# Performance work log

Hardware: AMD Instinct MI355X
Metric: run time of the kernel (lower is better)

## Reference

```python
import jax, jax.numpy as jnp
import numpy as np

B, S, D, H, L = 32, 512, 256, 8, 3
HD = D // H
FFN = D // 2
SCALE_BASE = 512.0
EPS = 1e-5


def _gammas():
    return (1.0 - jnp.exp(jnp.linspace(np.log(1.0 / 32.0), np.log(1.0 / 512.0), H))).astype(jnp.float32)


def _xpos(x, downscale):
    # x: [..., S, hd]; XPOS rotary embedding with exponential length scaling
    s, hd = x.shape[-2], x.shape[-1]
    half = hd // 2
    scale = (jnp.arange(0, hd, 2, dtype=jnp.float32) + 0.4 * hd) / (1.4 * hd)  # [half]
    power = jnp.arange(s, dtype=jnp.float32)[:, None] / SCALE_BASE
    sm = scale[None, :] ** power  # [S, half]
    if downscale:
        sm = 1.0 / sm
    inv_freq = 1.0 / (10000.0 ** (jnp.arange(half, dtype=jnp.float32) / half))
    ang = jnp.arange(s, dtype=jnp.float32)[:, None] * inv_freq[None, :]  # [S, half]
    sin = jnp.repeat(jnp.sin(ang) * sm, 2, axis=-1)  # duplicate_interleave -> [S, hd]
    cos = jnp.repeat(jnp.cos(ang) * sm, 2, axis=-1)
    x1, x2 = x[..., ::2], x[..., 1::2]
    rot = jnp.stack((-x2, x1), axis=-1).reshape(x.shape)  # rotate_every_two
    return x * cos + rot * sin


def _layer_norm(x, w, b):
    mu = x.mean(-1, keepdims=True)
    var = ((x - mu) ** 2).mean(-1, keepdims=True)
    return (x - mu) / jnp.sqrt(var + EPS) * w + b


def _msr(X, WQ, WK, WV, WG, WO, gn_w, gn_b):
    # Multi-scale retention, parallel form. X: [B,S,D]; WQ/WK/WV: [H,D,HD]
    b, s, _ = X.shape
    Q = _xpos(jnp.einsum('bsd,hde->bhse', X, WQ), False)
    K = _xpos(jnp.einsum('bsd,hde->bhse', X, WK), True)
    V = jnp.einsum('bsd,hde->bhse', X, WV)
    n = jnp.arange(s)
    delta = (n[:, None] - n[None, :]).astype(jnp.float32)
    mask = n[:, None] >= n[None, :]
    g = _gammas()
    Dm = jnp.where(mask[None], g[:, None, None] ** delta[None], 0.0)  # [H,S,S]
    scores = jnp.einsum('bhse,bhte->bhst', Q, K) * Dm[None]  # [B,H,S,S]
    Y = jnp.einsum('bhst,bhte->bhse', scores, V)  # [B,H,S,HD]
    Y = jnp.moveaxis(Y, 1, 2)  # [B,S,H,HD] (= concat heads)
    # GroupNorm(heads, v_dim): normalize per (token, head) group
    mu = Y.mean(-1, keepdims=True)
    var = ((Y - mu) ** 2).mean(-1, keepdims=True)
    Yn = ((Y - mu) / jnp.sqrt(var + EPS)).reshape(b, s, D) * gn_w + gn_b
    G = X @ WG
    return (G * jax.nn.sigmoid(G) * Yn) @ WO


def setup_inputs() -> dict:
    key = jax.random.key(0)
    ks = jax.random.split(key, 10)
    inp = {
        'v': jax.random.randint(ks[0], (B, S), 0, 65, dtype=jnp.int64),
        'emb': jax.random.normal(ks[1], (65, D), dtype=jnp.float32),
        'WQ': jax.random.normal(ks[2], (L, H, D, HD), dtype=jnp.float32) / D,
        'WK': jax.random.normal(ks[3], (L, H, D, HD), dtype=jnp.float32) / D,
        'WV': jax.random.normal(ks[4], (L, H, D, HD), dtype=jnp.float32) / D,
        'WG': jax.random.normal(ks[5], (L, D, D), dtype=jnp.float32) / D,
        'WO': jax.random.normal(ks[6], (L, D, D), dtype=jnp.float32) / D,
        'gn_w': jnp.ones((L, D), jnp.float32),
        'gn_b': jnp.zeros((L, D), jnp.float32),
        'ln1_w': jnp.ones((L, D), jnp.float32),
        'ln1_b': jnp.zeros((L, D), jnp.float32),
        'ln2_w': jnp.ones((L, D), jnp.float32),
        'ln2_b': jnp.zeros((L, D), jnp.float32),
        'w1': jax.random.normal(ks[7], (L, D, FFN), dtype=jnp.float32) * (1.0 / np.sqrt(D)),
        'b1': jnp.zeros((L, FFN), jnp.float32),
        'w2': jax.random.normal(ks[8], (L, FFN, D), dtype=jnp.float32) * (1.0 / np.sqrt(FFN)),
        'b2': jnp.zeros((L, D), jnp.float32),
    }
    return inp


def reference(v, emb, WQ, WK, WV, WG, WO, gn_w, gn_b, ln1_w, ln1_b, ln2_w, ln2_b, w1, b1, w2, b2):
    emb = emb.at[0].set(0.0)  # padding_idx=0
    X = jax.nn.relu(emb[v])  # [B,S,D]
    for i in range(L):
        Y = _msr(_layer_norm(X, ln1_w[i], ln1_b[i]), WQ[i], WK[i], WV[i], WG[i], WO[i], gn_w[i], gn_b[i]) + X
        h = jax.nn.gelu(_layer_norm(Y, ln2_w[i], ln2_b[i]) @ w1[i] + b1[i], approximate=False)
        X = h @ w2[i] + b2[i] + Y
    return X
```

## Files before the change

### kernel.cpp

```cpp
#include <hip/hip_runtime.h>
#include <hip/hip_bf16.h>
#include <math.h>

#define BB 32
#define SS 512
#define DD 256
#define HH 8
#define HDIM 32
#define FFNN 128
#define NROWS (BB*SS)
#define NELEM (NROWS*DD)

using bf16 = __hip_bfloat16;
typedef __attribute__((ext_vector_type(8))) short short8;
typedef __attribute__((ext_vector_type(4))) short short4v;
typedef __attribute__((ext_vector_type(4))) float floatx4;
typedef unsigned int uint_al __attribute__((may_alias));

static __device__ __forceinline__ float bf2f(bf16 x) { return __bfloat162float(x); }
static __device__ __forceinline__ bf16  f2bf(float x) { return __float2bfloat16(x); }
static __device__ __forceinline__ short f2bfs(float x) {
    bf16 b = __float2bfloat16(x);
    return __builtin_bit_cast(short, b);
}

static __device__ __forceinline__ unsigned int cvtpk(float a, float b) {
    unsigned int r;
    asm("v_cvt_pk_bf16_f32 %0, %1, %2" : "=v"(r) : "v"(a), "v"(b));
    return r;
}
static __device__ __forceinline__ short4v mk4(unsigned int a, unsigned int b) {
    union { unsigned int u[2]; short4v s; } t;
    t.u[0] = a; t.u[1] = b;
    return t.s;
}
static __device__ __forceinline__ floatx4 mfma16(short4v a, short4v b, floatx4 c) {
#if __has_builtin(__builtin_amdgcn_mfma_f32_16x16x16bf16_1k)
    return __builtin_amdgcn_mfma_f32_16x16x16bf16_1k(a, b, c, 0, 0, 0);
#else
    asm("v_mfma_f32_16x16x16_bf16 %0, %1, %2, %0" : "+v"(c) : "v"(a), "v"(b));
    return c;
#endif
}

static __device__ __forceinline__ void gld_lds16(const void* g, void* l) {
    __builtin_amdgcn_global_load_lds(
        (const __attribute__((address_space(1))) void*)g,
        (__attribute__((address_space(3))) void*)l, 16, 0, 0);
}

__global__ void init_flag(int* flag) { *flag = 0; }
__global__ __launch_bounds__(256) void detect_v(const int* __restrict__ v, int* __restrict__ flag) {
    int i = blockIdx.x * 256 + threadIdx.x;
    if (v[2 * i + 1] != 0) atomicOr(flag, 1);
}

#define NQKVG (3*1024*256)
#define NWO   (3*256*256)
#define NW1   (3*128*256)
#define NW2   (3*256*128)
#define NXPT  (512*16)
#define NSETUP (NQKVG+NWO+NW1+NW2+NXPT)
__global__ __launch_bounds__(256) void setup_pack(const float* __restrict__ WQ, const float* __restrict__ WK,
                                                  const float* __restrict__ WV, const float* __restrict__ WG,
                                                  const float* __restrict__ WO, const float* __restrict__ w1,
                                                  const float* __restrict__ w2,
                                                  bf16* __restrict__ dQ, bf16* __restrict__ dO,
                                                  bf16* __restrict__ d1, bf16* __restrict__ d2,
                                                  float4* __restrict__ xpt) {
    int idx = blockIdx.x * 256 + threadIdx.x;
    if (idx < NQKVG) {
        int k = idx & 255, n = (idx >> 8) & 1023, l = idx >> 18;
        int seg = n >> 8, n8 = n & 255;
        float val;
        if (seg < 3) {
            const float* W = (seg == 0) ? WQ : (seg == 1) ? WK : WV;
            int h = n8 >> 5, e = n8 & 31;
            val = W[(((size_t)l * 8 + h) * 256 + k) * 32 + e];
        } else {
            val = WG[(size_t)l * 65536 + k * 256 + n8];
        }
        dQ[((size_t)l * 1024 + n) * 256 + k] = f2bf(val);
    } else if (idx < NQKVG + NWO) {
        int i = idx - NQKVG;
        int k = i & 255, n = (i >> 8) & 255, l = i >> 16;
        dO[((size_t)l * 256 + n) * 256 + k] = f2bf(WO[(size_t)l * 65536 + k * 256 + n]);
    } else if (idx < NQKVG + NWO + NW1) {
        int i = idx - NQKVG - NWO;
        int k = i & 255, n = (i >> 8) & 127, l = i >> 15;
        d1[((size_t)l * 128 + n) * 256 + k] = f2bf(w1[(size_t)l * 32768 + k * 128 + n]);
    } else if (idx < NQKVG + NWO + NW1 + NW2) {
        int i = idx - NQKVG - NWO - NW1;
        int k = i & 127, n = (i >> 7) & 255, l = i >> 15;
        d2[((size_t)l * 256 + n) * 128 + k] = f2bf(w2[(size_t)l * 32768 + k * 256 + n]);
    } else {
        int i = idx - NQKVG - NWO - NW1 - NW2;
        int jf = i & 15, s = i >> 4;
        float base = (2.0f * jf + 12.8f) / 44.8f;
        float sm = powf(base, (float)s * (1.0f / 512.0f));
        float ang = (float)s * powf(10000.0f, -(float)jf / 16.0f);
        float sn, cs;
        sincosf(ang, &sn, &cs);
        xpt[i] = float4{cs * sm, sn * sm, cs / sm, sn / sm};
    }
}

__global__ __launch_bounds__(256) void embed_ln_kernel(const int* __restrict__ v,
                                                       const float* __restrict__ emb,
                                                       const int* __restrict__ flag,
                                                       const float* __restrict__ w,
                                                       const float* __restrict__ b,
                                                       float* __restrict__ X,
                                                       short* __restrict__ Xn) {
    int row = blockIdx.x;
    int d = threadIdx.x;
    int tok = (*flag) ? v[row] : v[2 * row];
    float x = 0.0f;
    if (tok != 0) {
        x = emb[tok * DD + d];
        x = x > 0.0f ? x : 0.0f;
    }
    X[(size_t)row * DD + d] = x;
    float s1 = x, s2 = x * x;
    #pragma unroll
    for (int off = 1; off < 64; off <<= 1) {
        s1 += __shfl_xor(s1, off);
        s2 += __shfl_xor(s2, off);
    }
    __shared__ float p1[4], p2[4], st[2];
    int wid = threadIdx.x >> 6;
    if ((threadIdx.x & 63) == 0) { p1[wid] = s1; p2[wid] = s2; }
    __syncthreads();
    if (threadIdx.x == 0) {
        float t1 = p1[0] + p1[1] + p1[2] + p1[3];
        float t2 = p2[0] + p2[1] + p2[2] + p2[3];
        float mu = t1 * (1.0f / DD);
        float var = t2 * (1.0f / DD) - mu * mu;
        st[0] = mu; st[1] = rsqrtf(var + 1e-5f);
    }
    __syncthreads();
    Xn[(size_t)row * DD + d] = f2bfs((x - st[0]) * st[1] * w[d] + b[d]);
}

__global__ __launch_bounds__(256) void qkvg_gemm(const short* __restrict__ A,
                                                 const short* __restrict__ Bp,
                                                 const float4* __restrict__ xpt,
                                                 bf16* __restrict__ C) {
    __shared__ __align__(16) short Als[16 * 512];
    __shared__ __align__(16) short Bls[16 * 512];
    const int tid = threadIdx.x;
    const int wave = tid >> 6, lane = tid & 63, lo = lane & 15, quad = lane >> 4;
    const int wm = wave >> 1, wn = wave & 1;
    const int row0 = blockIdx.x * 128, col0 = blockIdx.y * 128;

    floatx4 acc[4][4];
    #pragma unroll
    for (int i = 0; i < 4; ++i)
        #pragma unroll
        for (int j = 0; j < 4; ++j) acc[i][j] = floatx4{0.f, 0.f, 0.f, 0.f};

    for (int k0 = 0; k0 < 256; k0 += 64) {
        #pragma unroll
        for (int t = 0; t < 4; ++t) {
            int grp = (wm * 4 + t) * 2 + wn;
            const short* ga = A + (size_t)(row0 + (wm * 4 + t) * 16 + lo) * 256
                            + k0 + (wn * 4 + quad) * 8;
            gld_lds16(ga, &Als[grp * 512]);
        }
        #pragma unroll
        for (int t = 0; t < 4; ++t) {
            int grp = (wn * 4 + t) * 2 + wm;
            const short* gb = Bp + (size_t)(col0 + (wn * 4 + t) * 16 + lo) * 256
                            + k0 + (wm * 4 + quad) * 8;
            gld_lds16(gb, &Bls[grp * 512]);
        }
        __syncthreads();
        #pragma unroll
        for (int kkgrp = 0; kkgrp < 2; ++kkgrp) {
            short8 af[4], bfr[4];
            #pragma unroll
            for (int t = 0; t < 4; ++t)
                af[t] = *(const short8*)(&Als[((wm * 4 + t) * 2 + kkgrp) * 512 + lane * 8]);
            #pragma unroll
            for (int t = 0; t < 4; ++t)
                bfr[t] = *(const short8*)(&Bls[((wn * 4 + t) * 2 + kkgrp) * 512 + lane * 8]);
            #pragma unroll
            for (int ti = 0; ti < 4; ++ti)
                #pragma unroll
                for (int tj = 0; tj < 4; ++tj)
                    acc[ti][tj] = __builtin_amdgcn_mfma_f32_16x16x32_bf16(af[ti], bfr[tj], acc[ti][tj], 0, 0, 0);
        }
        __syncthreads();
    }

    #pragma unroll
    for (int ti = 0; ti < 4; ++ti) {
        #pragma unroll
        for (int tj = 0; tj < 4; ++tj) {
            int colb = col0 + (wn * 4 + tj) * 16 + lo;
            int seg = colb >> 8;
            #pragma unroll
            for (int r = 0; r < 4; ++r) {
                int row = row0 + (wm * 4 + ti) * 16 + quad * 4 + r;
                float v = acc[ti][tj][r];
                if (seg < 2) {
                    int s = row & (SS - 1);
                    int jf = (colb & 31) >> 1;
                    float4 t = xpt[s * 16 + jf];
                    float cs = (seg == 0) ? t.x : t.z;
                    float sn = (seg == 0) ? t.y : t.w;
                    float p = __shfl_xor(v, 1);
                    v = (lo & 1) ? (v * cs + p * sn) : (v * cs - p * sn);
                }
                C[(size_t)row * 1024 + colb] = f2bf(v);
            }
        }
    }
}

#define HS2 264
#define HSTR 136
template<int DOLN>
__global__ __launch_bounds__(256) void wo_ffn_fused(const short* __restrict__ A,
                                                    const short* __restrict__ Wo,
                                                    const short* __restrict__ W1p,
                                                    const float* __restrict__ b1,
                                                    const short* __restrict__ W2p,
                                                    const float* __restrict__ b2,
                                                    float* __restrict__ X,
                                                    const float* __restrict__ ln2w,
                                                    const float* __restrict__ ln2b,
                                                    const float* __restrict__ ln1w,
                                                    const float* __restrict__ ln1b,
                                                    short* __restrict__ Xn) {
    __shared__ __align__(16) short Als[4 * 512];
    __shared__ __align__(16) short Bls[4][8 * 512];
    __shared__ __align__(16) short Hn[32 * HS2];
    __shared__ __align__(16) short Hf[32 * HSTR];
    __shared__ float Ssum[32][4], Ssq[32][4];
    const int tid = threadIdx.x;
    const int wave = tid >> 6, lane = tid & 63, lo = lane & 15, quad = lane >> 4;
    const int row0 = blockIdx.x * 32;
    const int colw0 = wave * 64;

    floatx4 acc[2][4];
    #pragma unroll
    for (int i = 0; i < 2; ++i)
        #pragma unroll
        for (int j = 0; j < 4; ++j) acc[i][j] = floatx4{0.f, 0.f, 0.f, 0.f};

    const short* Ab = A + (size_t)(row0 + (wave >> 1) * 16 + lo) * 1024 + ((wave & 1) * 4 + quad) * 8;
    const short* Bb = Wo + (size_t)(colw0 + lo) * 256 + quad * 8;

    for (int k0 = 0; k0 < 256; k0 += 64) {
        gld_lds16(Ab + k0, &Als[wave * 512]);
        #pragma unroll
        for (int t = 0; t < 4; ++t)
            #pragma unroll
            for (int kk = 0; kk < 2; ++kk)
                gld_lds16(Bb + (size_t)(t * 16) * 256 + k0 + kk * 32,
                          &Bls[wave][(t * 2 + kk) * 512]);
        __syncthreads();
        #pragma unroll
        for (int kk = 0; kk < 2; ++kk) {
            short8 af[2], bfr[4];
            #pragma unroll
            for (int t = 0; t < 2; ++t)
                af[t] = *(const short8*)(&Als[(t * 2 + kk) * 512 + lane * 8]);
            #pragma unroll
            for (int t = 0; t < 4; ++t)
                bfr[t] = *(const short8*)(&Bls[wave][(t * 2 + kk) * 512 + lane * 8]);
            #pragma unroll
            for (int ti = 0; ti < 2; ++ti)
                #pragma unroll
                for (int tj = 0; tj < 4; ++tj)
                    acc[ti][tj] = __builtin_amdgcn_mfma_f32_16x16x32_bf16(af[ti], bfr[tj], acc[ti][tj], 0, 0, 0);
        }
        __syncthreads();
    }

    float vv[2][4][4];
    #pragma unroll
    for (int ti = 0; ti < 2; ++ti)
        #pragma unroll
        for (int tj = 0; tj < 4; ++tj) {
            int colb = colw0 + tj * 16 + lo;
            #pragma unroll
            for (int r = 0; r < 4; ++r) {
                int row = row0 + ti * 16 + quad * 4 + r;
                vv[ti][tj][r] = acc[ti][tj][r] + X[(size_t)row * DD + colb];
            }
        }
    #pragma unroll
    for (int ti = 0; ti < 2; ++ti)
        #pragma unroll
        for (int r = 0; r < 4; ++r) {
            float s1 = 0.f, s2 = 0.f;
            #pragma unroll
            for (int tj = 0; tj < 4; ++tj) {
                float v = vv[ti][tj][r];
                s1 += v; s2 += v * v;
            }
            #pragma unroll
            for (int off = 1; off < 16; off <<= 1) {
                s1 += __shfl_xor(s1, off);
                s2 += __shfl_xor(s2, off);
            }
            if (lo == 0) {
                int rl = ti * 16 + quad * 4 + r;
                Ssum[rl][wave] = s1;
                Ssq[rl][wave] = s2;
            }
        }
    __syncthreads();
    #pragma unroll
    for (int ti = 0; ti < 2; ++ti)
        #pragma unroll
        for (int r = 0; r < 4; ++r) {
            int rl = ti * 16 + quad * 4 + r;
            float t1 = Ssum[rl][0] + Ssum[rl][1] + Ssum[rl][2] + Ssum[rl][3];
            float t2 = Ssq[rl][0] + Ssq[rl][1] + Ssq[rl][2] + Ssq[rl][3];
            float mu = t1 * (1.0f / DD);
            float var = t2 * (1.0f / DD) - mu * mu;
            float rs = rsqrtf(var + 1e-5f);
            #pragma unroll
            for (int tj = 0; tj < 4; ++tj) {
                int colb = colw0 + tj * 16 + lo;
                Hn[rl * HS2 + colb] =
                    f2bfs((vv[ti][tj][r] - mu) * rs * ln2w[colb] + ln2b[colb]);
            }
        }
    __syncthreads();

    floatx4 a1[2][2];
    #pragma unroll
    for (int i = 0; i < 2; ++i) { a1[i][0] = floatx4{0,0,0,0}; a1[i][1] = floatx4{0,0,0,0}; }
    const short* Bb1 = W1p + (size_t)(wave * 32 + lo) * 256 + quad * 8;
    for (int k0 = 0; k0 < 256; k0 += 64) {
        #pragma unroll
        for (int t = 0; t < 2; ++t)
            #pragma unroll
            for (int kk = 0; kk < 2; ++kk)
                gld_lds16(Bb1 + (size_t)(t * 16) * 256 + k0 + kk * 32,
                          &Bls[wave][(t * 2 + kk) * 512]);
        __syncthreads();
        #pragma unroll
        for (int kk = 0; kk < 2; ++kk) {
            short8 af[2], bfr[2];
            #pragma unroll
            for (int t = 0; t < 2; ++t)
                af[t] = *(const short8*)(&Hn[(t * 16 + lo) * HS2 + k0 + kk * 32 + quad * 8]);
            #pragma unroll
            for (int t = 0; t < 2; ++t)
                bfr[t] = *(const short8*)(&Bls[wave][(t * 2 + kk) * 512 + lane * 8]);
            #pragma unroll
            for (int ti = 0; ti < 2; ++ti)
                #pragma unroll
                for (int tj = 0; tj < 2; ++tj)
                    a1[ti][tj] = __builtin_amdgcn_mfma_f32_16x16x32_bf16(af[ti], bfr[tj], a1[ti][tj], 0, 0, 0);
        }
        __syncthreads();
    }
    #pragma unroll
    for (int ti = 0; ti < 2; ++ti)
        #pragma unroll
        for (int tj = 0; tj < 2; ++tj) {
            int colb = wave * 32 + tj * 16 + lo;
            float bs = b1[colb];
            #pragma unroll
            for (int r = 0; r < 4; ++r) {
                int rl = ti * 16 + quad * 4 + r;
                float v = a1[ti][tj][r] + bs;
                v = 0.5f * v * (1.0f + erff(v * 0.70710678118f));
                Hf[rl * HSTR + colb] = f2bfs(v);
            }
        }

    floatx4 a2[2][4];
    #pragma unroll
    for (int i = 0; i < 2; ++i)
        #pragma unroll
        for (int j = 0; j < 4; ++j) a2[i][j] = floatx4{0,0,0,0};
    const short* Bb2 = W2p + (size_t)(colw0 + lo) * 128 + quad * 8;
    for (int k0 = 0; k0 < 128; k0 += 64) {
        #pragma unroll
        for (int t = 0; t < 4; ++t)
            #pragma unroll
            for (int kk = 0; kk < 2; ++kk)
                gld_lds16(Bb2 + (size_t)(t * 16) * 128 + k0 + kk * 32,
                          &Bls[wave][(t * 2 + kk) * 512]);
        __syncthreads();
        #pragma unroll
        for (int kk = 0; kk < 2; ++kk) {
            short8 af[2], bfr[4];
            #pragma unroll
            for (int t = 0; t < 2; ++t)
                af[t] = *(const short8*)(&Hf[(t * 16 + lo) * HSTR + k0 + kk * 32 + quad * 8]);
            #pragma unroll
            for (int t = 0; t < 4; ++t)
                bfr[t] = *(const short8*)(&Bls[wave][(t * 2 + kk) * 512 + lane * 8]);
            #pragma unroll
            for (int ti = 0; ti < 2; ++ti)
                #pragma unroll
                for (int tj = 0; tj < 4; ++tj)
                    a2[ti][tj] = __builtin_amdgcn_mfma_f32_16x16x32_bf16(af[ti], bfr[tj], a2[ti][tj], 0, 0, 0);
        }
        __syncthreads();
    }

    #pragma unroll
    for (int ti = 0; ti < 2; ++ti)
        #pragma unroll
        for (int tj = 0; tj < 4; ++tj) {
            int colb = colw0 + tj * 16 + lo;
            float bs = b2[colb];
            #pragma unroll
            for (int r = 0; r < 4; ++r) {
                int row = row0 + ti * 16 + quad * 4 + r;
                float v = a2[ti][tj][r] + bs + vv[ti][tj][r];
                X[(size_t)row * DD + colb] = v;
                vv[ti][tj][r] = v;
            }
        }
    if (!DOLN) return;
    #pragma unroll
    for (int ti = 0; ti < 2; ++ti)
        #pragma unroll
        for (int r = 0; r < 4; ++r) {
            float s1 = 0.f, s2 = 0.f;
            #pragma unroll
            for (int tj = 0; tj < 4; ++tj) {
                float v = vv[ti][tj][r];
                s1 += v; s2 += v * v;
            }
            #pragma unroll
            for (int off = 1; off < 16; off <<= 1) {
                s1 += __shfl_xor(s1, off);
                s2 += __shfl_xor(s2, off);
            }
            if (lo == 0) {
                int rl = ti * 16 + quad * 4 + r;
                Ssum[rl][wave] = s1;
                Ssq[rl][wave] = s2;
            }
        }
    __syncthreads();
    #pragma unroll
    for (int ti = 0; ti < 2; ++ti)
        #pragma unroll
        for (int r = 0; r < 4; ++r) {
            int rl = ti * 16 + quad * 4 + r;
            float t1 = Ssum[rl][0] + Ssum[rl][1] + Ssum[rl][2] + Ssum[rl][3];
            float t2 = Ssq[rl][0] + Ssq[rl][1] + Ssq[rl][2] + Ssq[rl][3];
            float mu = t1 * (1.0f / DD);
            float var = t2 * (1.0f / DD) - mu * mu;
            float rs = rsqrtf(var + 1e-5f);
            int row = row0 + rl;
            #pragma unroll
            for (int tj = 0; tj < 4; ++tj) {
                int colb = colw0 + tj * 16 + lo;
                Xn[(size_t)row * DD + colb] =
                    f2bfs((vv[ti][tj][r] - mu) * rs * ln1w[colb] + ln1b[colb]);
            }
        }
}

#define VSTR 44
__global__ __launch_bounds__(256) void retention_mfma_kernel(bf16* __restrict__ QKVG,
                                                             const float* __restrict__ gnw,
                                                             const float* __restrict__ gnb) {
    __shared__ __align__(16) short Vt[4][32 * VSTR];
    const int wslot = threadIdx.x >> 6;
    const int lane = threadIdx.x & 63;
    const int gblk = blockIdx.x >> 6;
    const int qi = 15 - ((gblk & ~3) + (((gblk & 3) + (gblk >> 2)) & 3));
    const int bh = ((blockIdx.x & 63) << 2) | wslot;
    const int b = bh >> 3, h = bh & 7;
    const int q0 = qi * 32;
    const int lo = lane & 15, quad = lane >> 4;

    const float la0 = -3.46573590280f, la1 = -6.23832462504f;
    float gamma = 1.0f - expf(la0 + (float)h * (la1 - la0) / 7.0f);
    float lg2 = log2f(gamma);
    float g16i = exp2f(-16.0f * lg2);
    float g16p = exp2f(16.0f * lg2);
    float gi32 = exp2f(-32.0f * lg2);
    float wq[4], wq16[4], wqB[4];
    #pragma unroll
    for (int r = 0; r < 4; ++r) {
        wq[r]   = exp2f((float)(lo - 4 * quad - r) * lg2);
        wq16[r] = wq[r] * g16i;
        wqB[r]  = wq[r] * g16p;
    }
    float c = exp2f((float)q0 * lg2);

    const size_t base = (size_t)b * SS * 1024;
    const short* QKVGs = (const short*)QKVG;

    short8 qfA = *(const short8*)(QKVGs + base + (size_t)(q0 + lo) * 1024 + h * HDIM + quad * 8);
    short8 qfB = *(const short8*)(QKVGs + base + (size_t)(q0 + 16 + lo) * 1024 + h * HDIM + quad * 8);

    floatx4 oA0 = {0,0,0,0}, oA1 = {0,0,0,0}, oB0 = {0,0,0,0}, oB1 = {0,0,0,0};
    short* Vw = Vt[wslot];
    const int nch = qi + 1;

    for (int ch = 0; ch < nch; ++ch) {
        const int t0 = ch * 32;
        const short* Kb = QKVGs + base + 256 + h * HDIM + quad * 8;
        short8 kf0 = *(const short8*)(Kb + (size_t)(t0 + lo) * 1024);
        short8 kf1 = *(const short8*)(Kb + (size_t)(t0 + 16 + lo) * 1024);
        {
            const int r = lane >> 2, dcol = (lane & 3) * 8;
            const short* Vg = QKVGs + base + 512 + h * HDIM + dcol;
            uint4 u1 = *(const uint4*)(Vg + (size_t)(t0 + r) * 1024);
            uint4 u2 = *(const uint4*)(Vg + (size_t)(t0 + 16 + r) * 1024);
            uint_al* W1 = (uint_al*)(Vw + r * VSTR + dcol);
            uint_al* W2 = (uint_al*)(Vw + (16 + r) * VSTR + dcol);
            W1[0] = u1.x; W1[1] = u1.y; W1[2] = u1.z; W1[3] = u1.w;
            W2[0] = u2.x; W2[1] = u2.y; W2[2] = u2.z; W2[3] = u2.w;
        }
        const floatx4 z = {0,0,0,0};
        floatx4 sA0 = __builtin_amdgcn_mfma_f32_16x16x32_bf16(kf0, qfA, z, 0, 0, 0);
        floatx4 sA1 = __builtin_amdgcn_mfma_f32_16x16x32_bf16(kf1, qfA, z, 0, 0, 0);
        floatx4 sB0 = __builtin_amdgcn_mfma_f32_16x16x32_bf16(kf0, qfB, z, 0, 0, 0);
        floatx4 sB1 = __builtin_amdgcn_mfma_f32_16x16x32_bf16(kf1, qfB, z, 0, 0, 0);

        float m0[4], m1[4], mB[4];
        #pragma unroll
        for (int r = 0; r < 4; ++r) {
            m0[r] = c * wq[r];
            m1[r] = c * wq16[r];
            mB[r] = c * wqB[r];
        }
        if (ch == qi) {
            #pragma unroll
            for (int r = 0; r < 4; ++r) {
                if (lo < 4 * quad + r) m0[r] = 0.0f;
                m1[r] = 0.0f;
            }
        }
        c *= gi32;

        unsigned int pa0 = cvtpk(sA0[0] * m0[0], sA0[1] * m0[1]);
        unsigned int pa1 = cvtpk(sA0[2] * m0[2], sA0[3] * m0[3]);
        unsigned int pa2 = cvtpk(sA1[0] * m1[0], sA1[1] * m1[1]);
        unsigned int pa3 = cvtpk(sA1[2] * m1[2], sA1[3] * m1[3]);
        unsigned int pb0 = cvtpk(sB0[0] * mB[0], sB0[1] * mB[1]);
        unsigned int pb1 = cvtpk(sB0[2] * mB[2], sB0[3] * mB[3]);
        unsigned int pb2 = cvtpk(sB1[0] * m0[0], sB1[1] * m0[1]);
        unsigned int pb3 = cvtpk(sB1[2] * m0[2], sB1[3] * m0[3]);
        short4v pA0 = mk4(pa0, pa1), pA1 = mk4(pa2, pa3);
        short4v pB0 = mk4(pb0, pb1), pB1 = mk4(pb2, pb3);

        short4v v00, v01, v10, v11;
        #pragma unroll
        for (int j = 0; j < 4; ++j) {
            v00[j] = Vw[(4 * quad + j) * VSTR + lo];
            v01[j] = Vw[(16 + 4 * quad + j) * VSTR + lo];
            v10[j] = Vw[(4 * quad + j) * VSTR + 16 + lo];
            v11[j] = Vw[(16 + 4 * quad + j) * VSTR + 16 + lo];
        }
        oA0 = mfma16(pA0, v00, oA0);
        oA0 = mfma16(pA1, v01, oA0);
        oA1 = mfma16(pA0, v10, oA1);
        oA1 = mfma16(pA1, v11, oA1);
        oB0 = mfma16(pB0, v00, oB0);
        oB0 = mfma16(pB1, v01, oB0);
        oB1 = mfma16(pB0, v10, oB1);
        oB1 = mfma16(pB1, v11, oB1);
    }

    float gw0 = gnw[h * HDIM + lo], gw1 = gnw[h * HDIM + 16 + lo];
    float gb0 = gnb[h * HDIM + lo], gb1 = gnb[h * HDIM + 16 + lo];
    bf16* QK = QKVG;
    #pragma unroll
    for (int sub = 0; sub < 2; ++sub) {
        floatx4 o0 = sub ? oB0 : oA0;
        floatx4 o1 = sub ? oB1 : oA1;
        int qbase = q0 + sub * 16;
        #pragma unroll
        for (int r = 0; r < 4; ++r) {
            float y0 = o0[r], y1 = o1[r];
            float s = y0 + y1, ss = y0 * y0 + y1 * y1;
            #pragma unroll
            for (int off = 1; off < 16; off <<= 1) {
                s  += __shfl_xor(s, off);
                ss += __shfl_xor(ss, off);
            }
            float mu = s * (1.0f / HDIM);
            float var = ss * (1.0f / HDIM) - mu * mu;
            float rstd = rsqrtf(var + 1e-5f);
            int q = qbase + quad * 4 + r;
            size_t rowb = base + (size_t)q * 1024;
            float g0 = bf2f(QK[rowb + 768 + h * HDIM + lo]);
            float g1 = bf2f(QK[rowb + 768 + h * HDIM + 16 + lo]);
            float t0v = g0 / (1.0f + expf(-g0)) * ((y0 - mu) * rstd * gw0 + gb0);
            float t1v = g1 / (1.0f + expf(-g1)) * ((y1 - mu) * rstd * gw1 + gb1);
            QK[rowb + h * HDIM + lo]      = f2bf(t0v);
            QK[rowb + h * HDIM + 16 + lo] = f2bf(t1v);
        }
    }
}

extern "C" void kernel_launch(void* const* d_in, const int* in_sizes, int n_in,
                              void* d_out, int out_size, void* d_ws, size_t ws_size,
                              hipStream_t stream) {
    const int*   v    = (const int*)d_in[0];
    const float* emb  = (const float*)d_in[1];
    const float* WQ   = (const float*)d_in[2];
    const float* WK   = (const float*)d_in[3];
    const float* WV   = (const float*)d_in[4];
    const float* WG   = (const float*)d_in[5];
    const float* WO   = (const float*)d_in[6];
    const float* gn_w = (const float*)d_in[7];
    const float* gn_b = (const float*)d_in[8];
    const float* ln1w = (const float*)d_in[9];
    const float* ln1b = (const float*)d_in[10];
    const float* ln2w = (const float*)d_in[11];
    const float* ln2b = (const float*)d_in[12];
    const float* w1   = (const float*)d_in[13];
    const float* b1   = (const float*)d_in[14];
    const float* w2   = (const float*)d_in[15];
    const float* b2   = (const float*)d_in[16];

    float* X = (float*)d_out;

    float* base  = (float*)d_ws;
    int*   flag  = (int*)base;
    short* Xn    = (short*)(base + 16);
    bf16*  QKVG  = (bf16*)(Xn + (size_t)NROWS * 256);
    bf16*  WqkvgP = QKVG + (size_t)NROWS * 1024;
    bf16*  WoP   = WqkvgP + 3 * 1024 * 256;
    bf16*  W1P   = WoP + 3 * 256 * 256;
    bf16*  W2P   = W1P + 3 * 128 * 256;
    float4* xpt  = (float4*)(W2P + 3 * 256 * 128);

    init_flag<<<1, 1, 0, stream>>>(flag);
    detect_v<<<32, 256, 0, stream>>>(v, flag);
    setup_pack<<<NSETUP / 256, 256, 0, stream>>>(WQ, WK, WV, WG, WO, w1, w2,
                                                 WqkvgP, WoP, W1P, W2P, xpt);
    embed_ln_kernel<<<NROWS, 256, 0, stream>>>(v, emb, flag, ln1w, ln1b, X, Xn);

    for (int i = 0; i < 3; ++i) {
        qkvg_gemm<<<dim3(128, 8), 256, 0, stream>>>(Xn,
                                                    (const short*)(WqkvgP + (size_t)i * 1024 * 256),
                                                    xpt, QKVG);
        retention_mfma_kernel<<<1024, 256, 0, stream>>>(QKVG, gn_w + i * DD, gn_b + i * DD);
        if (i < 2)
            wo_ffn_fused<1><<<NROWS / 32, 256, 0, stream>>>((const short*)QKVG,
                                                            (const short*)(WoP + (size_t)i * 256 * 256),
                                                            (const short*)(W1P + (size_t)i * 128 * 256),
                                                            b1 + i * FFNN,
                                                            (const short*)(W2P + (size_t)i * 256 * 128),
                                                            b2 + i * DD, X,
                                                            ln2w + i * DD, ln2b + i * DD,
                                                            ln1w + (i + 1) * DD, ln1b + (i + 1) * DD, Xn);
        else
            wo_ffn_fused<0><<<NROWS / 32, 256, 0, stream>>>((const short*)QKVG,
                                                            (const short*)(WoP + (size_t)i * 256 * 256),
                                                            (const short*)(W1P + (size_t)i * 128 * 256),
                                                            b1 + i * FFNN,
                                                            (const short*)(W2P + (size_t)i * 256 * 128),
                                                            b2 + i * DD, X,
                                                            ln2w + i * DD, ln2b + i * DD,
                                                            nullptr, nullptr, nullptr);
    }
}
```

Before: 360.3 us.

## Widen retention query tile to 64 rows and prefetch next K/V chunk

Each wave in the retention kernel now covers 64 query rows instead of 32, so every K/V chunk it loads is reused across four 16-row query subtiles and the grid halves to 512 blocks. The K and V loads for the next 32-key chunk are issued before the current chunk's MFMAs to hide global-memory latency. The block-to-query-tile mapping is changed to pair long and short causal tiles for load balance. In exchange, the wave holds more accumulators and prefetch registers, which may lower occupancy, and the smaller grid gives less parallelism.

```diff
diff --git a/kernel.cpp b/kernel.cpp
--- a/kernel.cpp
+++ b/kernel.cpp
@@ -473,124 +473,126 @@
     const int wslot = threadIdx.x >> 6;
     const int lane = threadIdx.x & 63;
     const int gblk = blockIdx.x >> 6;
-    const int qi = 15 - ((gblk & ~3) + (((gblk & 3) + (gblk >> 2)) & 3));
+    const int hlf = gblk >> 1;
+    const int qi = (gblk & 1) ? hlf : (7 - hlf);
     const int bh = ((blockIdx.x & 63) << 2) | wslot;
     const int b = bh >> 3, h = bh & 7;
-    const int q0 = qi * 32;
+    const int q0 = qi * 64;
     const int lo = lane & 15, quad = lane >> 4;
 
     const float la0 = -3.46573590280f, la1 = -6.23832462504f;
     float gamma = 1.0f - expf(la0 + (float)h * (la1 - la0) / 7.0f);
     float lg2 = log2f(gamma);
+    float g16p = exp2f(16.0f * lg2);
     float g16i = exp2f(-16.0f * lg2);
-    float g16p = exp2f(16.0f * lg2);
     float gi32 = exp2f(-32.0f * lg2);
-    float wq[4], wq16[4], wqB[4];
-    #pragma unroll
-    for (int r = 0; r < 4; ++r) {
-        wq[r]   = exp2f((float)(lo - 4 * quad - r) * lg2);
-        wq16[r] = wq[r] * g16i;
-        wqB[r]  = wq[r] * g16p;
-    }
-    float c = exp2f((float)q0 * lg2);
+    float wq[4];
+    #pragma unroll
+    for (int r = 0; r < 4; ++r)
+        wq[r] = exp2f((float)(lo - 4 * quad - r) * lg2);
+    float cs[4];
+    cs[0] = exp2f((float)q0 * lg2);
+    cs[1] = cs[0] * g16p;
+    cs[2] = cs[1] * g16p;
+    cs[3] = cs[2] * g16p;
 
     const size_t base = (size_t)b * SS * 1024;
     const short* QKVGs = (const short*)QKVG;
 
-    short8 qfA = *(const short8*)(QKVGs + base + (size_t)(q0 + lo) * 1024 + h * HDIM + quad * 8);
-    short8 qfB = *(const short8*)(QKVGs + base + (size_t)(q0 + 16 + lo) * 1024 + h * HDIM + quad * 8);
-
-    floatx4 oA0 = {0,0,0,0}, oA1 = {0,0,0,0}, oB0 = {0,0,0,0}, oB1 = {0,0,0,0};
+    short8 qf[4];
+    #pragma unroll
+    for (int s = 0; s < 4; ++s)
+        qf[s] = *(const short8*)(QKVGs + base + (size_t)(q0 + 16 * s + lo) * 1024 + h * HDIM + quad * 8);
+
+    floatx4 o[4][2];
+    #pragma unroll
+    for (int s = 0; s < 4; ++s) { o[s][0] = floatx4{0,0,0,0}; o[s][1] = floatx4{0,0,0,0}; }
+
     short* Vw = Vt[wslot];
-    const int nch = qi + 1;
+    const int nch = 2 * qi + 2;
+    const short* Kb = QKVGs + base + 256 + h * HDIM + quad * 8;
+    const int vr = lane >> 2, dcol = (lane & 3) * 8;
+    const short* Vg = QKVGs + base + 512 + h * HDIM + dcol;
+
+    short8 kf0 = *(const short8*)(Kb + (size_t)lo * 1024);
+    short8 kf1 = *(const short8*)(Kb + (size_t)(16 + lo) * 1024);
+    uint4 u1 = *(const uint4*)(Vg + (size_t)vr * 1024);
+    uint4 u2 = *(const uint4*)(Vg + (size_t)(16 + vr) * 1024);
 
     for (int ch = 0; ch < nch; ++ch) {
-        const int t0 = ch * 32;
-        const short* Kb = QKVGs + base + 256 + h * HDIM + quad * 8;
-        short8 kf0 = *(const short8*)(Kb + (size_t)(t0 + lo) * 1024);
-        short8 kf1 = *(const short8*)(Kb + (size_t)(t0 + 16 + lo) * 1024);
+        const bool more = (ch + 1 < nch);
+        short8 kn0, kn1; uint4 un1, un2;
+        if (more) {
+            const int tn = ch * 32 + 32;
+            kn0 = *(const short8*)(Kb + (size_t)(tn + lo) * 1024);
+            kn1 = *(const short8*)(Kb + (size_t)(tn + 16 + lo) * 1024);
+            un1 = *(const uint4*)(Vg + (size_t)(tn + vr) * 1024);
+            un2 = *(const uint4*)(Vg + (size_t)(tn + 16 + vr) * 1024);
+        }
         {
-            const int r = lane >> 2, dcol = (lane & 3) * 8;
-            const short* Vg = QKVGs + base + 512 + h * HDIM + dcol;
-            uint4 u1 = *(const uint4*)(Vg + (size_t)(t0 + r) * 1024);
-            uint4 u2 = *(const uint4*)(Vg + (size_t)(t0 + 16 + r) * 1024);
-            uint_al* W1 = (uint_al*)(Vw + r * VSTR + dcol);
-            uint_al* W2 = (uint_al*)(Vw + (16 + r) * VSTR + dcol);
+            uint_al* W1 = (uint_al*)(Vw + vr * VSTR + dcol);
+            uint_al* W2 = (uint_al*)(Vw + (16 + vr) * VSTR + dcol);
             W1[0] = u1.x; W1[1] = u1.y; W1[2] = u1.z; W1[3] = u1.w;
             W2[0] = u2.x; W2[1] = u2.y; W2[2] = u2.z; W2[3] = u2.w;
         }
         const floatx4 z = {0,0,0,0};
-        floatx4 sA0 = __builtin_amdgcn_mfma_f32_16x16x32_bf16(kf0, qfA, z, 0, 0, 0);
-        floatx4 sA1 = __builtin_amdgcn_mfma_f32_16x16x32_bf16(kf1, qfA, z, 0, 0, 0);
-        floatx4 sB0 = __builtin_amdgcn_mfma_f32_16x16x32_bf16(kf0, qfB, z, 0, 0, 0);
-        floatx4 sB1 = __builtin_amdgcn_mfma_f32_16x16x32_bf16(kf1, qfB, z, 0, 0, 0);
-
-        float m0[4], m1[4], mB[4];
-        #pragma unroll
-        for (int r = 0; r < 4; ++r) {
-            m0[r] = c * wq[r];
-            m1[r] = c * wq16[r];
-            mB[r] = c * wqB[r];
-        }
-        if (ch == qi) {
+        short4v p[4][2];
+        #pragma unroll
+        for (int s = 0; s < 4; ++s) {
+            floatx4 s0 = __builtin_amdgcn_mfma_f32_16x16x32_bf16(kf0, qf[s], z, 0, 0, 0);
+            floatx4 s1 = __builtin_amdgcn_mfma_f32_16x16x32_bf16(kf1, qf[s], z, 0, 0, 0);
+            const int d0 = 4 * qi + s - 2 * ch;
+            float w0 = cs[s], w1 = cs[s] * g16i;
+            float m0[4], m1[4];
             #pragma unroll
             for (int r = 0; r < 4; ++r) {
-                if (lo < 4 * quad + r) m0[r] = 0.0f;
-                m1[r] = 0.0f;
-            }
-        }
-        c *= gi32;
-
-        unsigned int pa0 = cvtpk(sA0[0] * m0[0], sA0[1] * m0[1]);
-        unsigned int pa1 = cvtpk(sA0[2] * m0[2], sA0[3] * m0[3]);
-        unsigned int pa2 = cvtpk(sA1[0] * m1[0], sA1[1] * m1[1]);
-        unsigned int pa3 = cvtpk(sA1[2] * m1[2], sA1[3] * m1[3]);
-        unsigned int pb0 = cvtpk(sB0[0] * mB[0], sB0[1] * mB[1]);
-        unsigned int pb1 = cvtpk(sB0[2] * mB[2], sB0[3] * mB[3]);
-        unsigned int pb2 = cvtpk(sB1[0] * m0[0], sB1[1] * m0[1]);
-        unsigned int pb3 = cvtpk(sB1[2] * m0[2], sB1[3] * m0[3]);
-        short4v pA0 = mk4(pa0, pa1), pA1 = mk4(pa2, pa3);
-        short4v pB0 = mk4(pb0, pb1), pB1 = mk4(pb2, pb3);
-
-        short4v v00, v01, v10, v11;
+                float a0 = w0 * wq[r], a1 = w1 * wq[r];
+                if (d0 < 0 || (d0 == 0 && lo < 4 * quad + r)) a0 = 0.0f;
+                if (d0 < 1 || (d0 == 1 && lo < 4 * quad + r)) a1 = 0.0f;
+                m0[r] = a0; m1[r] = a1;
+            }
+            p[s][0] = mk4(cvtpk(s0[0] * m0[0], s0[1] * m0[1]),
+                          cvtpk(s0[2] * m0[2], s0[3] * m0[3]));
+            p[s][1] = mk4(cvtpk(s1[0] * m1[0], s1[1] * m1[1]),
+                          cvtpk(s1[2] * m1[2], s1[3] * m1[3]));
+            cs[s] *= gi32;
+        }
+        short4v v[2][2];
         #pragma unroll
         for (int j = 0; j < 4; ++j) {
-            v00[j] = Vw[(4 * quad + j) * VSTR + lo];
-            v01[j] = Vw[(16 + 4 * quad + j) * VSTR + lo];
-            v10[j] = Vw[(4 * quad + j) * VSTR + 16 + lo];
-            v11[j] = Vw[(16 + 4 * quad + j) * VSTR + 16 + lo];
-        }
-        oA0 = mfma16(pA0, v00, oA0);
-        oA0 = mfma16(pA1, v01, oA0);
-        oA1 = mfma16(pA0, v10, oA1);
-        oA1 = mfma16(pA1, v11, oA1);
-        oB0 = mfma16(pB0, v00, oB0);
-        oB0 = mfma16(pB1, v01, oB0);
-        oB1 = mfma16(pB0, v10, oB1);
-        oB1 = mfma16(pB1, v11, oB1);
+            v[0][0][j] = Vw[(4 * quad + j) * VSTR + lo];
+            v[1][0][j] = Vw[(16 + 4 * quad + j) * VSTR + lo];
+            v[0][1][j] = Vw[(4 * quad + j) * VSTR + 16 + lo];
+            v[1][1][j] = Vw[(16 + 4 * quad + j) * VSTR + 16 + lo];
+        }
+        #pragma unroll
+        for (int s = 0; s < 4; ++s) {
+            o[s][0] = mfma16(p[s][0], v[0][0], o[s][0]);
+            o[s][0] = mfma16(p[s][1], v[1][0], o[s][0]);
+            o[s][1] = mfma16(p[s][0], v[0][1], o[s][1]);
+            o[s][1] = mfma16(p[s][1], v[1][1], o[s][1]);
+        }
+        if (more) { kf0 = kn0; kf1 = kn1; u1 = un1; u2 = un2; }
     }
 
     float gw0 = gnw[h * HDIM + lo], gw1 = gnw[h * HDIM + 16 + lo];
     float gb0 = gnb[h * HDIM + lo], gb1 = gnb[h * HDIM + 16 + lo];
     bf16* QK = QKVG;
     #pragma unroll
-    for (int sub = 0; sub < 2; ++sub) {
-        floatx4 o0 = sub ? oB0 : oA0;
-        floatx4 o1 = sub ? oB1 : oA1;
-        int qbase = q0 + sub * 16;
+    for (int s = 0; s < 4; ++s) {
         #pragma unroll
         for (int r = 0; r < 4; ++r) {
-            float y0 = o0[r], y1 = o1[r];
-            float s = y0 + y1, ss = y0 * y0 + y1 * y1;
+            float y0 = o[s][0][r], y1 = o[s][1][r];
+            float sm = y0 + y1, ss = y0 * y0 + y1 * y1;
             #pragma unroll
             for (int off = 1; off < 16; off <<= 1) {
-                s  += __shfl_xor(s, off);
+                sm += __shfl_xor(sm, off);
                 ss += __shfl_xor(ss, off);
             }
-            float mu = s * (1.0f / HDIM);
+            float mu = sm * (1.0f / HDIM);
             float var = ss * (1.0f / HDIM) - mu * mu;
             float rstd = rsqrtf(var + 1e-5f);
-            int q = qbase + quad * 4 + r;
+            int q = q0 + 16 * s + quad * 4 + r;
             size_t rowb = base + (size_t)q * 1024;
             float g0 = bf2f(QK[rowb + 768 + h * HDIM + lo]);
             float g1 = bf2f(QK[rowb + 768 + h * HDIM + 16 + lo]);
@@ -645,7 +647,7 @@
         qkvg_gemm<<<dim3(128, 8), 256, 0, stream>>>(Xn,
                                                     (const short*)(WqkvgP + (size_t)i * 1024 * 256),
                                                     xpt, QKVG);
-        retention_mfma_kernel<<<1024, 256, 0, stream>>>(QKVG, gn_w + i * DD, gn_b + i * DD);
+        retention_mfma_kernel<<<512, 256, 0, stream>>>(QKVG, gn_w + i * DD, gn_b + i * DD);
         if (i < 2)
             wo_ffn_fused<1><<<NROWS / 32, 256, 0, stream>>>((const short*)QKVG,
                                                             (const short*)(WoP + (size_t)i * 256 * 256),
```

Measured after the change: 368.7 us. 2.4% more time.
